# Performance work log

Hardware: AMD Instinct MI355X
Metric: run time of the kernel (lower is better)

Reference implementation:

```python
import jax, jax.numpy as jnp
import numpy as np
from jax import lax

KERNEL = 21
SHIFT = KERNEL - 1  # 20
NUM_LEVELS = 2
EPS = 1e-5
NEG_SLOPE = 0.01


def _conv1d(x, w):
    # x: [B, Cin, T], w: [Cout, Cin, K] -> [B, Cout, T-K+1]
    return lax.conv_general_dilated(x, w, window_strides=(1,), padding='VALID',
                                    dimension_numbers=('NCH', 'OIH', 'NCH'))


def _batchnorm_train(x, gamma, beta):
    # training-mode BN over (N, L) per channel, biased variance (torch semantics)
    mean = jnp.mean(x, axis=(0, 2), keepdims=True)
    var = jnp.mean((x - mean) ** 2, axis=(0, 2), keepdims=True)
    return (x - mean) * lax.rsqrt(var + EPS) * gamma[None, :, None] + beta[None, :, None]


def _spp(y, L, num_levels, pool):
    # y: [B, C, Tc]; L: [B] valid lengths. Level i has 2^i bins:
    #   bin j covers [j*floor(L/2^i), j*floor(L/2^i)+ceil(L/2^i)), matching
    #   F.max_pool1d/avg_pool1d(kernel=ceil(f), stride=floor(f)) on x[:, :, :L].
    B, C, Tc = y.shape
    pos = jnp.arange(Tc)[None, :]                     # [1, Tc]
    Lf = L.astype(jnp.float32)
    outs = []
    for i in range(num_levels):
        k = 2 ** i
        f = Lf / k
        stride = jnp.floor(f).astype(jnp.int32)        # [B]
        kern = jnp.ceil(f).astype(jnp.int32)           # [B]
        bins = []
        for j in range(k):
            start = j * stride                         # [B]
            mask = (pos >= start[:, None]) & (pos < (start + kern)[:, None])  # [B, Tc]
            m = mask[:, None, :]                       # [B, 1, Tc]
            if pool == 'max':
                bins.append(jnp.max(jnp.where(m, y, -jnp.inf), axis=-1))      # [B, C]
            else:
                s = jnp.sum(jnp.where(m, y, jnp.zeros((), y.dtype)), axis=-1)
                bins.append(s / kern[:, None].astype(y.dtype))
        # torch .view flattens (C, k) channel-major
        outs.append(jnp.stack(bins, axis=-1).reshape(B, C * k))
    return jnp.concatenate(outs, axis=1)               # [B, C*(2^n - 1)]


def setup_inputs() -> dict:
    key = jax.random.key(0)
    k1, k2, k3, k4, k5 = jax.random.split(key, 5)
    B, C, T = 32, 64, 16384
    n_tasks = 2
    n_lin = 2 * C * (2 ** NUM_LEVELS - 1)  # 384
    x = jax.random.normal(k1, (B, C, T), dtype=jnp.float32)
    orig_len = jax.random.randint(k2, (B,), T // 2, T + 1, dtype=jnp.int32)
    w1 = jax.random.normal(k3, (C, C, KERNEL), dtype=jnp.float32) * 0.05
    w2 = jax.random.normal(k4, (C, C, KERNEL), dtype=jnp.float32) * 0.05
    g1 = jnp.ones((C,), jnp.float32); b1 = jnp.zeros((C,), jnp.float32)
    g2 = jnp.ones((C,), jnp.float32); b2 = jnp.zeros((C,), jnp.float32)
    fc_w = jax.random.normal(k5, (n_tasks, n_lin), dtype=jnp.float32) * 0.05
    fc_b = jnp.zeros((n_tasks,), jnp.float32)
    return {"x": x, "orig_len": orig_len, "w1": w1, "g1": g1, "b1": b1,
            "w2": w2, "g2": g2, "b2": b2, "fc_w": fc_w, "fc_b": fc_b}


def reference(x, orig_len, w1, g1, b1, w2, g2, b2, fc_w, fc_b):
    L = orig_len - SHIFT  # valid conv-output length per sample
    y1 = jax.nn.leaky_relu(_batchnorm_train(_conv1d(x, w1), g1, b1), NEG_SLOPE)
    p1 = _spp(y1, L, NUM_LEVELS, 'max')
    y2 = jax.nn.leaky_relu(_batchnorm_train(_conv1d(x, w2), g2, b2), NEG_SLOPE)
    p2 = _spp(y2, L, NUM_LEVELS, 'avg')
    feat = jnp.concatenate([p1, p2], axis=1)           # [B, 384]
    return feat @ fc_w.T + fc_b
```

## Files before the change

### kernel.cpp

```cpp
#include <hip/hip_runtime.h>

#define AS1 __attribute__((address_space(1)))
#define AS3 __attribute__((address_space(3)))

using u16 = unsigned short;
using u32 = unsigned int;
typedef __attribute__((ext_vector_type(8))) short bf16x8;
typedef __attribute__((ext_vector_type(4))) float f32x4;

constexpr int Bn    = 32;
constexpr int Tn    = 16384;
constexpr int TCn   = 16364;
constexpr int TILE  = 256;
constexpr int XROWS = 280;
constexpr int TPAD  = 16416;
constexpr int SPPCH = 64;

__device__ __forceinline__ u16 f2bf(float f) {
  union { float f; u32 u; } v; v.f = f;
  u32 u = v.u;
  u += 0x7fffu + ((u >> 16) & 1u);
  return (u16)(u >> 16);
}
__device__ __forceinline__ float bf2f(u32 h) {
  union { u32 u; float f; } v; v.u = h << 16; return v.f;
}
__device__ __forceinline__ u32 encf(float f) {
  union { float f; u32 u; } v; v.f = f;
  return (v.u & 0x80000000u) ? ~v.u : (v.u | 0x80000000u);
}
__device__ __forceinline__ float decf(u32 u) {
  union { u32 u; float f; } v;
  v.u = (u & 0x80000000u) ? (u ^ 0x80000000u) : ~u;
  return v.f;
}
__device__ __forceinline__ void gload_lds16(const void* g, void* l) {
  __builtin_amdgcn_global_load_lds((const AS1 u32*)g, (AS3 u32*)l, 16, 0, 0);
}
__device__ __forceinline__ float leaky(float z) { return z > 0.f ? z : 0.01f * z; }

__global__ __launch_bounds__(256) void transpose_x(const float* __restrict__ x,
                                                   u16* __restrict__ x_t,
                                                   const float* __restrict__ w1,
                                                   const float* __restrict__ w2,
                                                   u16* __restrict__ wf1,
                                                   u16* __restrict__ wf2) {
  __shared__ u16 lt[64][64];
  const int bx  = blockIdx.x;
  const int tid = threadIdx.x;

  if (bx >= Bn * 256) {
    const int bxx = bx - Bn * 256;
    const int cv  = bxx / 42;
    const int c   = bxx % 42;
    const float* w = cv ? w2 : w1;
    u16* wf = cv ? wf2 : wf1;
    const int ct   = tid >> 6;
    const int lane = tid & 63;
    const int q  = lane >> 4;
    const int rr = lane & 15;
    const int k  = c >> 1;
    const int cb = (c & 1) * 32;
    const int co = ct * 16 + rr;
    u16 us[8] __attribute__((aligned(16)));
#pragma unroll
    for (int j = 0; j < 8; ++j) {
      int ci = cb + q * 8 + j;
      us[j] = f2bf(w[((size_t)co * 64 + ci) * 21 + k]);
    }
    *(uint4*)&wf[((size_t)(c * 4 + ct) * 64 + lane) * 8] = *(const uint4*)us;
    return;
  }

  const int b   = bx >> 8;
  const int tt  = bx & 255;
  const int t0  = tt * 64;
  const int ci0 = (tid & 15) * 4;
  const int tl0 = (tid >> 4) * 4;
  float4 v[4];
#pragma unroll
  for (int j = 0; j < 4; ++j)
    v[j] = *(const float4*)(x + (size_t)(b * 64 + ci0 + j) * Tn + t0 + tl0);
  float vr[4][4] = {{v[0].x,v[0].y,v[0].z,v[0].w},{v[1].x,v[1].y,v[1].z,v[1].w},
                    {v[2].x,v[2].y,v[2].z,v[2].w},{v[3].x,v[3].y,v[3].z,v[3].w}};
#pragma unroll
  for (int e = 0; e < 4; ++e) {
    int tl = tl0 + e;
    u32 lo = (u32)f2bf(vr[0][e]) | ((u32)f2bf(vr[1][e]) << 16);
    u32 hi = (u32)f2bf(vr[2][e]) | ((u32)f2bf(vr[3][e]) << 16);
    uint2 pk = make_uint2(lo, hi);
    *(uint2*)&lt[tl][ci0] = pk;
  }
  __syncthreads();
  const int row = tid >> 2;
  const int seg = tid & 3;
  const int c0  = seg * 16;
  const int sw  = (row & 7) * 8;
  u16* op = x_t + ((size_t)b * TPAD + t0 + row) * 64 + c0;
  *(uint4*)op       = *(const uint4*)&lt[row][c0 ^ sw];
  *(uint4*)(op + 8) = *(const uint4*)&lt[row][(c0 + 8) ^ sw];
  if (tt == 0) {
    uint4 z = make_uint4(0u, 0u, 0u, 0u);
    uint4* pz = (uint4*)(x_t + ((size_t)b * TPAD + Tn) * 64);
    pz[tid] = z;
  }
}

__global__ __launch_bounds__(256, 4) void conv_mfma(const u16* __restrict__ x_t,
                                                    const u16* __restrict__ wf1,
                                                    const u16* __restrict__ wf2,
                                                    u16* __restrict__ y1,
                                                    u16* __restrict__ y2,
                                                    float* __restrict__ stats) {
  __shared__ u16 xs[XROWS * 64];
  __shared__ float sred[128];

  const int bid  = blockIdx.x;
  const int cv   = bid & 1;
  const int tmp  = bid >> 1;
  const int tile = tmp & 63;
  const int b    = tmp >> 6;
  const int t0   = tile * TILE;
  const int tid  = threadIdx.x;
  const int w    = tid >> 6;
  const int lane = tid & 63;
  const int q    = lane >> 4;
  const int r    = lane & 15;
  const u16* wf  = cv ? wf2 : wf1;

  if (tid < 128) sred[tid] = 0.f;

  const u16* xg = x_t + ((size_t)b * TPAD + t0) * 64;
  for (int s = w; s < 35; s += 4)
    gload_lds16(xg + (size_t)s * 512 + lane * 8, &xs[s * 512]);

  const u16* wfl = wf + lane * 8;
  bf16x8 afA[4], afB[4];
#pragma unroll
  for (int ct = 0; ct < 4; ++ct) afA[ct] = *(const bf16x8*)(wfl + ct * 512);
#pragma unroll
  for (int ct = 0; ct < 4; ++ct) afB[ct] = *(const bf16x8*)(wfl + 2048 + ct * 512);

  __syncthreads();

  f32x4 acc[4][4];
#pragma unroll
  for (int a = 0; a < 4; ++a)
#pragma unroll
    for (int t = 0; t < 4; ++t)
      acc[a][t] = (f32x4){0.f, 0.f, 0.f, 0.f};

  const int rowbase = w * 64 + r;

  for (int j = 0; j < 21; ++j) {
    const int swl  = ((rowbase + j) & 7) * 8;
    const int cid0 = (q * 8) ^ swl;
    const int cid1 = cid0 ^ 32;
    {
      bf16x8 bx[4];
#pragma unroll
      for (int tt = 0; tt < 4; ++tt)
        bx[tt] = *(const bf16x8*)&xs[(rowbase + tt * 16 + j) * 64 + cid0];
      __builtin_amdgcn_s_setprio(1);
#pragma unroll
      for (int ct = 0; ct < 4; ++ct)
#pragma unroll
        for (int tt = 0; tt < 4; ++tt)
          acc[ct][tt] = __builtin_amdgcn_mfma_f32_16x16x32_bf16(afA[ct], bx[tt], acc[ct][tt], 0, 0, 0);
      __builtin_amdgcn_s_setprio(0);
      if (j < 20) {
        const u16* p = wfl + (size_t)(2 * j + 2) * 2048;
#pragma unroll
        for (int ct = 0; ct < 4; ++ct) afA[ct] = *(const bf16x8*)(p + ct * 512);
      }
    }
    {
      bf16x8 bx[4];
#pragma unroll
      for (int tt = 0; tt < 4; ++tt)
        bx[tt] = *(const bf16x8*)&xs[(rowbase + tt * 16 + j) * 64 + cid1];
      __builtin_amdgcn_s_setprio(1);
#pragma unroll
      for (int ct = 0; ct < 4; ++ct)
#pragma unroll
        for (int tt = 0; tt < 4; ++tt)
          acc[ct][tt] = __builtin_amdgcn_mfma_f32_16x16x32_bf16(afB[ct], bx[tt], acc[ct][tt], 0, 0, 0);
      __builtin_amdgcn_s_setprio(0);
      if (j < 20) {
        const u16* p = wfl + (size_t)(2 * j + 3) * 2048;
#pragma unroll
        for (int ct = 0; ct < 4; ++ct) afB[ct] = *(const bf16x8*)(p + ct * 512);
      }
    }
  }

  const bool full_t = (t0 + TILE <= TCn);
#pragma unroll
  for (int ct = 0; ct < 4; ++ct)
#pragma unroll
    for (int i = 0; i < 4; ++i) {
      float sv = 0.f, sq = 0.f;
      if (full_t) {
#pragma unroll
        for (int tt = 0; tt < 4; ++tt) {
          float v = acc[ct][tt][i];
          sv += v; sq += v * v;
        }
      } else {
#pragma unroll
        for (int tt = 0; tt < 4; ++tt) {
          int tg = t0 + w * 64 + tt * 16 + r;
          if (tg < TCn) {
            float v = acc[ct][tt][i];
            sv += v; sq += v * v;
          }
        }
      }
#pragma unroll
      for (int m = 1; m < 16; m <<= 1) {
        sv += __shfl_xor(sv, m, 64);
        sq += __shfl_xor(sq, m, 64);
      }
      if (r == 0) {
        int co = ct * 16 + q * 4 + i;
        atomicAdd(&sred[co * 2], sv);
        atomicAdd(&sred[co * 2 + 1], sq);
      }
    }

  __syncthreads();

  u16* ys = xs;
#pragma unroll
  for (int ct = 0; ct < 4; ++ct)
#pragma unroll
    for (int tt = 0; tt < 4; ++tt) {
      int tl = w * 64 + tt * 16 + r;
      int sw = (tl & 7) * 8;
      int co0 = (ct * 16 + q * 4) ^ sw;
      u32 lo = (u32)f2bf(acc[ct][tt][0]) | ((u32)f2bf(acc[ct][tt][1]) << 16);
      u32 hi = (u32)f2bf(acc[ct][tt][2]) | ((u32)f2bf(acc[ct][tt][3]) << 16);
      *(uint2*)&ys[tl * 64 + co0] = make_uint2(lo, hi);
    }
  __syncthreads();
  u16* yo = (cv ? y2 : y1) + ((size_t)b * Tn + t0) * 64;
#pragma unroll
  for (int m = 0; m < 8; ++m) {
    int flat = m * 256 + tid;
    int row  = flat >> 3;
    int c0   = (flat & 7) * 8;
    int sw   = (row & 7) * 8;
    *(uint4*)(yo + (size_t)row * 64 + c0) = *(const uint4*)&ys[row * 64 + (c0 ^ sw)];
  }
  if (tid < 128) atomicAdd(&stats[cv * 128 + tid], sred[tid]);
}

__global__ __launch_bounds__(256) void spp(const u16* __restrict__ y1,
                                           const u16* __restrict__ y2,
                                           const float* __restrict__ stats,
                                           const float* __restrict__ g1v,
                                           const float* __restrict__ b1v,
                                           const float* __restrict__ g2v,
                                           const float* __restrict__ b2v,
                                           const int* __restrict__ orig_len,
                                           u32* __restrict__ part) {
  __shared__ float lred[4][16][4][5];
  const int bx = blockIdx.x;
  const int b  = bx >> 6;
  const int ch = bx & 63;
  const int tid  = threadIdx.x;
  const int g    = tid & 15;
  const int trow = tid >> 4;
  const int wv   = tid >> 6;
  const int co0  = g * 4;
  const int L     = orig_len[b] - 20;
  const int str2  = L >> 1;
  const int kern2 = L - str2;
  const float Nf = 32.0f * 16364.0f;
  float a1[4], c1[4], a2[4], c2[4];
#pragma unroll
  for (int j = 0; j < 4; ++j) {
    int co = co0 + j;
    float s, sq, mean, var;
    s = stats[co * 2]; sq = stats[co * 2 + 1];
    mean = s / Nf; var = sq / Nf - mean * mean; if (var < 0.f) var = 0.f;
    a1[j] = g1v[co] * rsqrtf(var + 1e-5f);
    c1[j] = b1v[co] - mean * a1[j];
    s = stats[128 + co * 2]; sq = stats[128 + co * 2 + 1];
    mean = s / Nf; var = sq / Nf - mean * mean; if (var < 0.f) var = 0.f;
    a2[j] = g2v[co] * rsqrtf(var + 1e-5f);
    c2[j] = b2v[co] - mean * a2[j];
  }
  float m1[4] = {-3.4e38f,-3.4e38f,-3.4e38f,-3.4e38f};
  float m2[4] = {-3.4e38f,-3.4e38f,-3.4e38f,-3.4e38f};
  float s0[4] = {0,0,0,0}, sb0[4] = {0,0,0,0}, sb1[4] = {0,0,0,0};
  const int tbase = ch * 256;
  int tend = tbase + 256;
  if (tend > L) tend = L;
  const u16* p1 = y1 + (size_t)b * Tn * 64 + co0;
  const u16* p2 = y2 + (size_t)b * Tn * 64 + co0;

  auto body = [&](int t) {
    uint2 v1 = *(const uint2*)(p1 + (size_t)t * 64);
    uint2 v2 = *(const uint2*)(p2 + (size_t)t * 64);
    float f1[4] = { bf2f(v1.x & 0xffffu), bf2f(v1.x >> 16),
                    bf2f(v1.y & 0xffffu), bf2f(v1.y >> 16) };
    float f2[4] = { bf2f(v2.x & 0xffffu), bf2f(v2.x >> 16),
                    bf2f(v2.y & 0xffffu), bf2f(v2.y >> 16) };
    bool in0 = (t < kern2), in1 = (t >= str2);
#pragma unroll
    for (int j = 0; j < 4; ++j) {
      float z1 = leaky(fmaf(a1[j], f1[j], c1[j]));
      float z2 = leaky(fmaf(a2[j], f2[j], c2[j]));
      s0[j] += z2;
      if (in0) { m1[j] = fmaxf(m1[j], z1); sb0[j] += z2; }
      if (in1) { m2[j] = fmaxf(m2[j], z1); sb1[j] += z2; }
    }
  };

  if (tend == tbase + 256) {
#pragma unroll 4
    for (int it = 0; it < 16; ++it)
      body(tbase + trow + it * 16);
  } else {
    for (int t = tbase + trow; t < tend; t += 16)
      body(t);
  }

#pragma unroll
  for (int m = 16; m <= 32; m <<= 1) {
#pragma unroll
    for (int j = 0; j < 4; ++j) {
      m1[j]  = fmaxf(m1[j], __shfl_xor(m1[j], m, 64));
      m2[j]  = fmaxf(m2[j], __shfl_xor(m2[j], m, 64));
      s0[j]  += __shfl_xor(s0[j],  m, 64);
      sb0[j] += __shfl_xor(sb0[j], m, 64);
      sb1[j] += __shfl_xor(sb1[j], m, 64);
    }
  }
  if (((tid & 63) >> 4) == 0) {
#pragma unroll
    for (int j = 0; j < 4; ++j) {
      lred[wv][g][j][0] = m1[j];
      lred[wv][g][j][1] = m2[j];
      lred[wv][g][j][2] = s0[j];
      lred[wv][g][j][3] = sb0[j];
      lred[wv][g][j][4] = sb1[j];
    }
  }
  __syncthreads();
  if (tid < 64) {
    const int co = tid;
    const int g2 = co >> 2, j2 = co & 3;
    float fm1 = lred[0][g2][j2][0], fm2 = lred[0][g2][j2][1];
    float fs0 = lred[0][g2][j2][2], fb0 = lred[0][g2][j2][3], fb1v_ = lred[0][g2][j2][4];
#pragma unroll
    for (int k = 1; k < 4; ++k) {
      fm1 = fmaxf(fm1, lred[k][g2][j2][0]);
      fm2 = fmaxf(fm2, lred[k][g2][j2][1]);
      fs0 += lred[k][g2][j2][2];
      fb0 += lred[k][g2][j2][3];
      fb1v_ += lred[k][g2][j2][4];
    }
    u32* pp = part + (size_t)bx * 384;
    float* pf = (float*)pp;
    u32 e1 = encf(fm1), e2 = encf(fm2);
    pp[co]              = e1 > e2 ? e1 : e2;
    pp[64 + co * 2]     = e1;
    pp[64 + co * 2 + 1] = e2;
    pf[192 + co]         = fs0;
    pf[256 + co * 2]     = fb0;
    pf[256 + co * 2 + 1] = fb1v_;
  }
}

__global__ __launch_bounds__(384) void fc(const u32* __restrict__ part,
                                          const int* __restrict__ orig_len,
                                          const float* __restrict__ fc_w,
                                          const float* __restrict__ fc_b,
                                          float* __restrict__ out) {
  __shared__ float r0s[6], r1s[6];
  const int b = blockIdx.x;
  const int j = threadIdx.x;
  const int L = orig_len[b] - 20;
  const int kern2 = L - (L >> 1);
  const u32* pb = part + (size_t)b * 64 * 384;
  float fv;
  if (j < 192) {
    u32 vmax = 0u;
    for (int c = 0; c < 64; ++c) {
      u32 v = pb[(size_t)c * 384 + j];
      vmax = v > vmax ? v : vmax;
    }
    fv = decf(vmax);
  } else {
    const float* pf = (const float*)pb;
    float s = 0.f;
    for (int c = 0; c < 64; ++c) s += pf[(size_t)c * 384 + j];
    fv = (j < 256) ? s / (float)L : s / (float)kern2;
  }
  float a0 = fv * fc_w[j];
  float a1 = fv * fc_w[384 + j];
#pragma unroll
  for (int m = 1; m < 64; m <<= 1) {
    a0 += __shfl_xor(a0, m, 64);
    a1 += __shfl_xor(a1, m, 64);
  }
  const int wv = j >> 6, ln = j & 63;
  if (ln == 0) { r0s[wv] = a0; r1s[wv] = a1; }
  __syncthreads();
  if (j == 0) {
    float t0 = 0.f, t1 = 0.f;
#pragma unroll
    for (int k = 0; k < 6; ++k) { t0 += r0s[k]; t1 += r1s[k]; }
    out[b * 2]     = t0 + fc_b[0];
    out[b * 2 + 1] = t1 + fc_b[1];
  }
}

extern "C" void kernel_launch(void* const* d_in, const int* in_sizes, int n_in,
                              void* d_out, int out_size, void* d_ws, size_t ws_size,
                              hipStream_t stream) {
  const float* x        = (const float*)d_in[0];
  const int*   orig_len = (const int*)d_in[1];
  const float* w1  = (const float*)d_in[2];
  const float* g1  = (const float*)d_in[3];
  const float* b1  = (const float*)d_in[4];
  const float* w2  = (const float*)d_in[5];
  const float* g2  = (const float*)d_in[6];
  const float* b2  = (const float*)d_in[7];
  const float* fcw = (const float*)d_in[8];
  const float* fcb = (const float*)d_in[9];
  float* out = (float*)d_out;

  char* ws = (char*)d_ws;
  const size_t XT_BYTES = (size_t)Bn * TPAD * 64 * 2;
  const size_t Y_BYTES  = (size_t)Bn * Tn * 64 * 2;
  const size_t WF_BYTES = (size_t)42 * 4 * 64 * 8 * 2;
  size_t off = 0;
  u16* x_t = (u16*)(ws + off); off += XT_BYTES;
  u16* y1  = (u16*)(ws + off); off += Y_BYTES;
  u16* y2  = (u16*)(ws + off); off += Y_BYTES;
  u16* wf1 = (u16*)(ws + off); off += WF_BYTES;
  u16* wf2 = (u16*)(ws + off); off += WF_BYTES;
  float* stats = (float*)(ws + off);
  u32*   part  = (u32*)(ws + off + 1024);

  hipMemsetAsync(stats, 0, 1024, stream);
  transpose_x<<<Bn * 256 + 84, 256, 0, stream>>>(x, x_t, w1, w2, wf1, wf2);
  conv_mfma<<<Bn * 64 * 2, 256, 0, stream>>>(x_t, wf1, wf2, y1, y2, stats);
  spp<<<Bn * SPPCH, 256, 0, stream>>>(y1, y2, stats, g1, b1, g2, b2, orig_len, part);
  fc<<<Bn, 384, 0, stream>>>(part, orig_len, fcw, fcb, out);
  (void)in_sizes; (void)n_in; (void)out_size; (void)ws_size;
}
```

Baseline: 395.1 us.

## Compute both convolutions in one block to share the staged input tile

Each conv block now computes both weight sets (w1 and w2) against the same LDS-staged x tile instead of launching separate blocks per conv. This halves global reads of x_t into LDS and the LDS B-fragment reads per MFMA pair, and halves the grid. In exchange, accumulator and weight-fragment register use doubles, launch bounds drop to 2 waves per SIMD, and the epilogue serialises the two output writes through shared memory.

New measurement: 403.4 us. +2.1%, slower.

```diff
diff --git a/kernel.cpp b/kernel.cpp
--- a/kernel.cpp
+++ b/kernel.cpp
@@ -106,49 +106,52 @@
   }
 }
 
-__global__ __launch_bounds__(256, 4) void conv_mfma(const u16* __restrict__ x_t,
+__global__ __launch_bounds__(256, 2) void conv_mfma(const u16* __restrict__ x_t,
                                                     const u16* __restrict__ wf1,
                                                     const u16* __restrict__ wf2,
                                                     u16* __restrict__ y1,
                                                     u16* __restrict__ y2,
                                                     float* __restrict__ stats) {
   __shared__ u16 xs[XROWS * 64];
-  __shared__ float sred[128];
+  __shared__ float sred[256];
 
   const int bid  = blockIdx.x;
-  const int cv   = bid & 1;
-  const int tmp  = bid >> 1;
-  const int tile = tmp & 63;
-  const int b    = tmp >> 6;
+  const int tile = bid & 63;
+  const int b    = bid >> 6;
   const int t0   = tile * TILE;
   const int tid  = threadIdx.x;
   const int w    = tid >> 6;
   const int lane = tid & 63;
   const int q    = lane >> 4;
   const int r    = lane & 15;
-  const u16* wf  = cv ? wf2 : wf1;
-
-  if (tid < 128) sred[tid] = 0.f;
+
+  sred[tid] = 0.f;
 
   const u16* xg = x_t + ((size_t)b * TPAD + t0) * 64;
   for (int s = w; s < 35; s += 4)
     gload_lds16(xg + (size_t)s * 512 + lane * 8, &xs[s * 512]);
 
-  const u16* wfl = wf + lane * 8;
-  bf16x8 afA[4], afB[4];
-#pragma unroll
-  for (int ct = 0; ct < 4; ++ct) afA[ct] = *(const bf16x8*)(wfl + ct * 512);
-#pragma unroll
-  for (int ct = 0; ct < 4; ++ct) afB[ct] = *(const bf16x8*)(wfl + 2048 + ct * 512);
-
-  __syncthreads();
-
-  f32x4 acc[4][4];
+  const u16* w1l = wf1 + lane * 8;
+  const u16* w2l = wf2 + lane * 8;
+  bf16x8 afA1[4], afA2[4], afB1[4], afB2[4];
+#pragma unroll
+  for (int ct = 0; ct < 4; ++ct) {
+    afA1[ct] = *(const bf16x8*)(w1l + ct * 512);
+    afA2[ct] = *(const bf16x8*)(w2l + ct * 512);
+    afB1[ct] = *(const bf16x8*)(w1l + 2048 + ct * 512);
+    afB2[ct] = *(const bf16x8*)(w2l + 2048 + ct * 512);
+  }
+
+  __syncthreads();
+
+  f32x4 accA[4][4], accB[4][4];
 #pragma unroll
   for (int a = 0; a < 4; ++a)
 #pragma unroll
-    for (int t = 0; t < 4; ++t)
-      acc[a][t] = (f32x4){0.f, 0.f, 0.f, 0.f};
+    for (int t = 0; t < 4; ++t) {
+      accA[a][t] = (f32x4){0.f, 0.f, 0.f, 0.f};
+      accB[a][t] = (f32x4){0.f, 0.f, 0.f, 0.f};
+    }
 
   const int rowbase = w * 64 + r;
 
@@ -165,13 +168,19 @@
 #pragma unroll
       for (int ct = 0; ct < 4; ++ct)
 #pragma unroll
-        for (int tt = 0; tt < 4; ++tt)
-          acc[ct][tt] = __builtin_amdgcn_mfma_f32_16x16x32_bf16(afA[ct], bx[tt], acc[ct][tt], 0, 0, 0);
+        for (int tt = 0; tt < 4; ++tt) {
+          accA[ct][tt] = __builtin_amdgcn_mfma_f32_16x16x32_bf16(afA1[ct], bx[tt], accA[ct][tt], 0, 0, 0);
+          accB[ct][tt] = __builtin_amdgcn_mfma_f32_16x16x32_bf16(afA2[ct], bx[tt], accB[ct][tt], 0, 0, 0);
+        }
       __builtin_amdgcn_s_setprio(0);
       if (j < 20) {
-        const u16* p = wfl + (size_t)(2 * j + 2) * 2048;
-#pragma unroll
-        for (int ct = 0; ct < 4; ++ct) afA[ct] = *(const bf16x8*)(p + ct * 512);
+        const u16* p1 = w1l + (size_t)(2 * j + 2) * 2048;
+        const u16* p2 = w2l + (size_t)(2 * j + 2) * 2048;
+#pragma unroll
+        for (int ct = 0; ct < 4; ++ct) {
+          afA1[ct] = *(const bf16x8*)(p1 + ct * 512);
+          afA2[ct] = *(const bf16x8*)(p2 + ct * 512);
+        }
       }
     }
     {
@@ -183,76 +192,95 @@
 #pragma unroll
       for (int ct = 0; ct < 4; ++ct)
 #pragma unroll
-        for (int tt = 0; tt < 4; ++tt)
-          acc[ct][tt] = __builtin_amdgcn_mfma_f32_16x16x32_bf16(afB[ct], bx[tt], acc[ct][tt], 0, 0, 0);
+        for (int tt = 0; tt < 4; ++tt) {
+          accA[ct][tt] = __builtin_amdgcn_mfma_f32_16x16x32_bf16(afB1[ct], bx[tt], accA[ct][tt], 0, 0, 0);
+          accB[ct][tt] = __builtin_amdgcn_mfma_f32_16x16x32_bf16(afB2[ct], bx[tt], accB[ct][tt], 0, 0, 0);
+        }
       __builtin_amdgcn_s_setprio(0);
       if (j < 20) {
-        const u16* p = wfl + (size_t)(2 * j + 3) * 2048;
-#pragma unroll
-        for (int ct = 0; ct < 4; ++ct) afB[ct] = *(const bf16x8*)(p + ct * 512);
+        const u16* p1 = w1l + (size_t)(2 * j + 3) * 2048;
+        const u16* p2 = w2l + (size_t)(2 * j + 3) * 2048;
+#pragma unroll
+        for (int ct = 0; ct < 4; ++ct) {
+          afB1[ct] = *(const bf16x8*)(p1 + ct * 512);
+          afB2[ct] = *(const bf16x8*)(p2 + ct * 512);
+        }
       }
     }
   }
 
   const bool full_t = (t0 + TILE <= TCn);
-#pragma unroll
-  for (int ct = 0; ct < 4; ++ct)
-#pragma unroll
-    for (int i = 0; i < 4; ++i) {
-      float sv = 0.f, sq = 0.f;
-      if (full_t) {
-#pragma unroll
-        for (int tt = 0; tt < 4; ++tt) {
-          float v = acc[ct][tt][i];
-          sv += v; sq += v * v;
-        }
-      } else {
-#pragma unroll
-        for (int tt = 0; tt < 4; ++tt) {
-          int tg = t0 + w * 64 + tt * 16 + r;
-          if (tg < TCn) {
+  auto bnstats = [&](f32x4 (&acc)[4][4], int base) {
+#pragma unroll
+    for (int ct = 0; ct < 4; ++ct)
+#pragma unroll
+      for (int i = 0; i < 4; ++i) {
+        float sv = 0.f, sq = 0.f;
+        if (full_t) {
+#pragma unroll
+          for (int tt = 0; tt < 4; ++tt) {
             float v = acc[ct][tt][i];
             sv += v; sq += v * v;
           }
+        } else {
+#pragma unroll
+          for (int tt = 0; tt < 4; ++tt) {
+            int tg = t0 + w * 64 + tt * 16 + r;
+            if (tg < TCn) {
+              float v = acc[ct][tt][i];
+              sv += v; sq += v * v;
+            }
+          }
+        }
+#pragma unroll
+        for (int m = 1; m < 16; m <<= 1) {
+          sv += __shfl_xor(sv, m, 64);
+          sq += __shfl_xor(sq, m, 64);
+        }
+        if (r == 0) {
+          int co = ct * 16 + q * 4 + i;
+          atomicAdd(&sred[base + co * 2], sv);
+          atomicAdd(&sred[base + co * 2 + 1], sq);
         }
       }
-#pragma unroll
-      for (int m = 1; m < 16; m <<= 1) {
-        sv += __shfl_xor(sv, m, 64);
-        sq += __shfl_xor(sq, m, 64);
+  };
+  bnstats(accA, 0);
+  bnstats(accB, 128);
+
+  __syncthreads();
+
+  u16* ys = xs;
+  auto writeYs = [&](f32x4 (&acc)[4][4]) {
+#pragma unroll
+    for (int ct = 0; ct < 4; ++ct)
+#pragma unroll
+      for (int tt = 0; tt < 4; ++tt) {
+        int tl = w * 64 + tt * 16 + r;
+        int sw = (tl & 7) * 8;
+        int co0 = (ct * 16 + q * 4) ^ sw;
+        u32 lo = (u32)f2bf(acc[ct][tt][0]) | ((u32)f2bf(acc[ct][tt][1]) << 16);
+        u32 hi = (u32)f2bf(acc[ct][tt][2]) | ((u32)f2bf(acc[ct][tt][3]) << 16);
+        *(uint2*)&ys[tl * 64 + co0] = make_uint2(lo, hi);
       }
-      if (r == 0) {
-        int co = ct * 16 + q * 4 + i;
-        atomicAdd(&sred[co * 2], sv);
-        atomicAdd(&sred[co * 2 + 1], sq);
-      }
-    }
-
-  __syncthreads();
-
-  u16* ys = xs;
-#pragma unroll
-  for (int ct = 0; ct < 4; ++ct)
-#pragma unroll
-    for (int tt = 0; tt < 4; ++tt) {
-      int tl = w * 64 + tt * 16 + r;
-      int sw = (tl & 7) * 8;
-      int co0 = (ct * 16 + q * 4) ^ sw;
-      u32 lo = (u32)f2bf(acc[ct][tt][0]) | ((u32)f2bf(acc[ct][tt][1]) << 16);
-      u32 hi = (u32)f2bf(acc[ct][tt][2]) | ((u32)f2bf(acc[ct][tt][3]) << 16);
-      *(uint2*)&ys[tl * 64 + co0] = make_uint2(lo, hi);
-    }
-  __syncthreads();
-  u16* yo = (cv ? y2 : y1) + ((size_t)b * Tn + t0) * 64;
-#pragma unroll
-  for (int m = 0; m < 8; ++m) {
-    int flat = m * 256 + tid;
-    int row  = flat >> 3;
-    int c0   = (flat & 7) * 8;
-    int sw   = (row & 7) * 8;
-    *(uint4*)(yo + (size_t)row * 64 + c0) = *(const uint4*)&ys[row * 64 + (c0 ^ sw)];
-  }
-  if (tid < 128) atomicAdd(&stats[cv * 128 + tid], sred[tid]);
+  };
+  auto storeYo = [&](u16* yo) {
+#pragma unroll
+    for (int m = 0; m < 8; ++m) {
+      int flat = m * 256 + tid;
+      int row  = flat >> 3;
+      int c0   = (flat & 7) * 8;
+      int sw   = (row & 7) * 8;
+      *(uint4*)(yo + (size_t)row * 64 + c0) = *(const uint4*)&ys[row * 64 + (c0 ^ sw)];
+    }
+  };
+  writeYs(accA);
+  __syncthreads();
+  storeYo(y1 + ((size_t)b * Tn + t0) * 64);
+  __syncthreads();
+  writeYs(accB);
+  __syncthreads();
+  storeYo(y2 + ((size_t)b * Tn + t0) * 64);
+  atomicAdd(&stats[tid], sred[tid]);
 }
 
 __global__ __launch_bounds__(256) void spp(const u16* __restrict__ y1,
@@ -448,7 +476,7 @@
 
   hipMemsetAsync(stats, 0, 1024, stream);
   transpose_x<<<Bn * 256 + 84, 256, 0, stream>>>(x, x_t, w1, w2, wf1, wf2);
-  conv_mfma<<<Bn * 64 * 2, 256, 0, stream>>>(x_t, wf1, wf2, y1, y2, stats);
+  conv_mfma<<<Bn * 64, 256, 0, stream>>>(x_t, wf1, wf2, y1, y2, stats);
   spp<<<Bn * SPPCH, 256, 0, stream>>>(y1, y2, stats, g1, b1, g2, b2, orig_len, part);
   fc<<<Bn, 384, 0, stream>>>(part, orig_len, fcw, fcb, out);
   (void)in_sizes; (void)n_in; (void)out_size; (void)ws_size;
```
